# Optimization experiments

Measured on AMD Instinct MI355X. Metric: run time of the kernel, lower is better.

## Reference

```python
import jax, jax.numpy as jnp
import numpy as np

BATCH, NBITS = 32768, 512


def setup_inputs() -> dict:
    key = jax.random.key(0)
    raw = jax.random.randint(key, (BATCH, NBITS), 0, 2)
    bits = raw.astype(jnp.float32) * 2.0 - 1.0  # values in {-1, +1}
    return {"bits": bits}


def _joint_prob(b):
    # b in {0,1}, shape [B, N]. p_ij[i,j,m,n] = mean_b 1[b_i==m] * 1[b_j==n]
    B = b.shape[0]
    ind = jnp.stack([(b == 0.0), (b == 1.0)], axis=0).astype(b.dtype)  # [2, B, N]
    return jnp.einsum('mbi,nbj->ijmn', ind, ind) / B  # [N, N, 2, 2]


def reference(bits):
    b = bits / 2.0 + 0.5
    N = b.shape[1]
    p_ij = _joint_prob(b)
    p_i_pos = b.mean(axis=0)
    p_i = jnp.stack([1.0 - p_i_pos, p_i_pos], axis=-1)  # [N, 2]
    outer = p_i[:, None, :, None] * p_i[None, :, None, :]  # [N, N, 2, 2]
    ii = jnp.arange(N)
    tri = (ii[:, None] > ii[None, :])[:, :, None, None]  # triangle: keep i > j
    valid = tri & (p_ij > 0) & (p_i[:, None, :, None] > 0) & (p_i[None, :, None, :] > 0)
    safe_p = jnp.where(valid, p_ij, 1.0)
    safe_o = jnp.where(valid, outer, 1.0)
    terms = jnp.where(valid, safe_p * jnp.log(safe_p / safe_o), 0.0)
    cnt = valid.sum().astype(bits.dtype)
    return terms.sum() / cnt
```

## Files before the change

kernel.cpp:

```cpp
#include <hip/hip_runtime.h>
#include <stdint.h>

#define BATCH   32768
#define NBITS   512
#define NWORDS  512
#define NSLICE  32
#define SW      16
#define NTILE   36

typedef unsigned long long u64;

__global__ __launch_bounds__(256) void pack_kernel(const float* __restrict__ bits,
                                                   u64* __restrict__ packed,
                                                   double* __restrict__ lg,
                                                   int* __restrict__ c1) {
    const int gid = blockIdx.x * 256 + threadIdx.x;

    if (gid <= BATCH) lg[gid] = (gid > 0) ? log((double)gid) : 0.0;
    if (gid < NBITS) c1[gid] = 0;

    const int wv   = threadIdx.x >> 6;
    const int lane = threadIdx.x & 63;
    const int gw   = blockIdx.x * 4 + wv;
    const int w    = gw >> 2;
    const int q    = gw & 3;
    const int c0   = q * 128 + lane * 2;

    u64 m0 = 0, m1 = 0;
    const float* base = bits + (size_t)w * 64 * NBITS + c0;
#pragma unroll 16
    for (int r = 0; r < 64; ++r) {
        float2 v = *reinterpret_cast<const float2*>(base + (size_t)r * NBITS);
        const u64 b = 1ull << r;
        if (v.x > 0.0f) m0 |= b;
        if (v.y > 0.0f) m1 |= b;
    }
    ulonglong2 st; st.x = m0; st.y = m1;
    *reinterpret_cast<ulonglong2*>(&packed[(size_t)w * NBITS + c0]) = st;
}

__global__ __launch_bounds__(256) void gram_kernel(const u64* __restrict__ packed,
                                                   int* __restrict__ Cp,
                                                   int* __restrict__ c1) {
    __shared__ u64 ldsI[SW][64];
    __shared__ u64 ldsJ[SW][64];

    const int s = blockIdx.x & (NSLICE - 1);
    const int t = blockIdx.x >> 5;
    int bi = (int)((sqrtf(8.0f * (float)t + 1.0f) - 1.0f) * 0.5f);
    while ((bi + 1) * (bi + 2) / 2 <= t) ++bi;
    while (bi * (bi + 1) / 2 > t) --bi;
    const int bj = t - bi * (bi + 1) / 2;

    const int i0 = bi * 64, j0 = bj * 64;
    const int w0 = s * SW;
    const bool diag = (bi == bj);

    for (int q = threadIdx.x; q < SW * 32; q += 256) {
        const int wo = q >> 5, cp = (q & 31) * 2;
        const size_t g = (size_t)(w0 + wo) * NBITS;
        *reinterpret_cast<ulonglong2*>(&ldsI[wo][cp]) =
            *reinterpret_cast<const ulonglong2*>(&packed[g + i0 + cp]);
        if (!diag)
            *reinterpret_cast<ulonglong2*>(&ldsJ[wo][cp]) =
                *reinterpret_cast<const ulonglong2*>(&packed[g + j0 + cp]);
    }
    __syncthreads();

    const int tj2 = (threadIdx.x & 15) * 2;
    const int ti2 = (threadIdx.x >> 4) * 2;
    const u64 (*BJ)[64] = diag ? ldsI : ldsJ;

    int acc[4][4] = {};
#pragma unroll
    for (int w = 0; w < SW; ++w) {
        const u64 a0 = ldsI[w][ti2],      a1 = ldsI[w][ti2 + 1];
        const u64 a2 = ldsI[w][ti2 + 32], a3 = ldsI[w][ti2 + 33];
        const u64 b0 = BJ[w][tj2],        b1 = BJ[w][tj2 + 1];
        const u64 b2 = BJ[w][tj2 + 32],   b3 = BJ[w][tj2 + 33];
        acc[0][0] += __popcll(a0 & b0); acc[0][1] += __popcll(a0 & b1);
        acc[0][2] += __popcll(a0 & b2); acc[0][3] += __popcll(a0 & b3);
        acc[1][0] += __popcll(a1 & b0); acc[1][1] += __popcll(a1 & b1);
        acc[1][2] += __popcll(a1 & b2); acc[1][3] += __popcll(a1 & b3);
        acc[2][0] += __popcll(a2 & b0); acc[2][1] += __popcll(a2 & b1);
        acc[2][2] += __popcll(a2 & b2); acc[2][3] += __popcll(a2 & b3);
        acc[3][0] += __popcll(a3 & b0); acc[3][1] += __popcll(a3 & b1);
        acc[3][2] += __popcll(a3 & b2); acc[3][3] += __popcll(a3 & b3);
    }

    int* out = Cp + (size_t)s * NBITS * NBITS;
    const int io[4] = {ti2, ti2 + 1, ti2 + 32, ti2 + 33};
#pragma unroll
    for (int a = 0; a < 4; ++a) {
        const size_t row = (size_t)(i0 + io[a]) * NBITS + j0;
        *reinterpret_cast<int2*>(&out[row + tj2])      = make_int2(acc[a][0], acc[a][1]);
        *reinterpret_cast<int2*>(&out[row + tj2 + 32]) = make_int2(acc[a][2], acc[a][3]);
    }

    if (diag && ti2 == tj2) {
#pragma unroll
        for (int a = 0; a < 4; ++a)
            atomicAdd(&c1[i0 + io[a]], acc[a][a]);
    }
}

__global__ __launch_bounds__(256) void mi_kernel(const int* __restrict__ Cp,
                                                 const int* __restrict__ c1,
                                                 const double* __restrict__ lg,
                                                 double* __restrict__ bsum,
                                                 int* __restrict__ bcnt) {
    const double invB = 1.0 / (double)BATCH;
    const int i = blockIdx.x;
    const int ci = c1[i];
    const double lgB = lg[BATCH];
    double lsum = 0.0;
    int lcnt = 0;

#pragma unroll
    for (int half = 0; half < 2; ++half) {
        const int j = half * 256 + threadIdx.x;
        if (j < i) {
            int n11 = 0;
#pragma unroll
            for (int s = 0; s < NSLICE; ++s)
                n11 += Cp[(size_t)s * NBITS * NBITS + (size_t)i * NBITS + j];
            const int cj = c1[j];

            const int pim[2] = {BATCH - ci, ci};
            const int pjn[2] = {BATCH - cj, cj};
            const int nmn[2][2] = {{BATCH - ci - cj + n11, cj - n11},
                                   {ci - n11, n11}};
#pragma unroll
            for (int m = 0; m < 2; ++m)
#pragma unroll
                for (int n = 0; n < 2; ++n) {
                    const int c_mn = nmn[m][n];
                    if (c_mn > 0 && pim[m] > 0 && pjn[n] > 0) {
                        lsum += (double)c_mn * invB *
                                (lg[c_mn] + lgB - lg[pim[m]] - lg[pjn[n]]);
                        ++lcnt;
                    }
                }
        }
    }

    __shared__ double ssum[256];
    __shared__ int scnt[256];
    ssum[threadIdx.x] = lsum;
    scnt[threadIdx.x] = lcnt;
    __syncthreads();
    for (int off = 128; off > 0; off >>= 1) {
        if (threadIdx.x < off) {
            ssum[threadIdx.x] += ssum[threadIdx.x + off];
            scnt[threadIdx.x] += scnt[threadIdx.x + off];
        }
        __syncthreads();
    }
    if (threadIdx.x == 0) { bsum[blockIdx.x] = ssum[0]; bcnt[blockIdx.x] = scnt[0]; }
}

__global__ __launch_bounds__(256) void final_kernel(const double* __restrict__ bsum,
                                                    const int* __restrict__ bcnt,
                                                    float* __restrict__ out,
                                                    int nblocks) {
    __shared__ double ssum[256];
    __shared__ int scnt[256];
    double s = 0.0; int c = 0;
    for (int k = threadIdx.x; k < nblocks; k += 256) { s += bsum[k]; c += bcnt[k]; }
    ssum[threadIdx.x] = s;
    scnt[threadIdx.x] = c;
    __syncthreads();
    for (int off = 128; off > 0; off >>= 1) {
        if (threadIdx.x < off) {
            ssum[threadIdx.x] += ssum[threadIdx.x + off];
            scnt[threadIdx.x] += scnt[threadIdx.x + off];
        }
        __syncthreads();
    }
    if (threadIdx.x == 0) out[0] = (float)(ssum[0] / (double)scnt[0]);
}

extern "C" void kernel_launch(void* const* d_in, const int* in_sizes, int n_in,
                              void* d_out, int out_size, void* d_ws, size_t ws_size,
                              hipStream_t stream) {
    const float* bits = (const float*)d_in[0];
    char* ws = (char*)d_ws;
    u64*    packed = (u64*)ws;
    int*    Cp     = (int*)(ws + (2u << 20));
    double* lg     = (double*)(ws + (34u << 20));
    int*    c1     = (int*)(ws + (34u << 20) + (512u << 10));
    double* bsum   = (double*)(ws + (34u << 20) + (576u << 10));
    int*    bcnt   = (int*)(ws + (34u << 20) + (640u << 10));

    pack_kernel<<<512, 256, 0, stream>>>(bits, packed, lg, c1);
    gram_kernel<<<NTILE * NSLICE, 256, 0, stream>>>(packed, Cp, c1);
    mi_kernel<<<NBITS, 256, 0, stream>>>(Cp, c1, lg, bsum, bcnt);
    final_kernel<<<1, 256, 0, stream>>>(bsum, bcnt, (float*)d_out, NBITS);
}
```

Before: 43.55 us.

## Retile gram kernel to 32x32 single-wave blocks and fuse final reduction

```diff
diff --git a/kernel.cpp b/kernel.cpp
--- a/kernel.cpp
+++ b/kernel.cpp
@@ -4,20 +4,23 @@
 #define BATCH   32768
 #define NBITS   512
 #define NWORDS  512
-#define NSLICE  32
-#define SW      16
-#define NTILE   36
+#define NSLICE  16
+#define SW      32
+#define NT32    136
+#define MIGRID  512
 
 typedef unsigned long long u64;
 
 __global__ __launch_bounds__(256) void pack_kernel(const float* __restrict__ bits,
                                                    u64* __restrict__ packed,
                                                    double* __restrict__ lg,
-                                                   int* __restrict__ c1) {
+                                                   int* __restrict__ c1,
+                                                   int* __restrict__ done) {
     const int gid = blockIdx.x * 256 + threadIdx.x;
 
     if (gid <= BATCH) lg[gid] = (gid > 0) ? log((double)gid) : 0.0;
     if (gid < NBITS) c1[gid] = 0;
+    if (gid == NBITS) *done = 0;
 
     const int wv   = threadIdx.x >> 6;
     const int lane = threadIdx.x & 63;
@@ -39,25 +42,25 @@
     *reinterpret_cast<ulonglong2*>(&packed[(size_t)w * NBITS + c0]) = st;
 }
 
-__global__ __launch_bounds__(256) void gram_kernel(const u64* __restrict__ packed,
-                                                   int* __restrict__ Cp,
-                                                   int* __restrict__ c1) {
-    __shared__ u64 ldsI[SW][64];
-    __shared__ u64 ldsJ[SW][64];
+__global__ __launch_bounds__(64) void gram_kernel(const u64* __restrict__ packed,
+                                                  int* __restrict__ Cp,
+                                                  int* __restrict__ c1) {
+    __shared__ u64 ldsI[SW][32];
+    __shared__ u64 ldsJ[SW][32];
 
     const int s = blockIdx.x & (NSLICE - 1);
-    const int t = blockIdx.x >> 5;
+    const int t = blockIdx.x >> 4;
     int bi = (int)((sqrtf(8.0f * (float)t + 1.0f) - 1.0f) * 0.5f);
     while ((bi + 1) * (bi + 2) / 2 <= t) ++bi;
     while (bi * (bi + 1) / 2 > t) --bi;
     const int bj = t - bi * (bi + 1) / 2;
 
-    const int i0 = bi * 64, j0 = bj * 64;
+    const int i0 = bi * 32, j0 = bj * 32;
     const int w0 = s * SW;
     const bool diag = (bi == bj);
 
-    for (int q = threadIdx.x; q < SW * 32; q += 256) {
-        const int wo = q >> 5, cp = (q & 31) * 2;
+    for (int q = threadIdx.x; q < SW * 16; q += 64) {
+        const int wo = q >> 4, cp = (q & 15) * 2;
         const size_t g = (size_t)(w0 + wo) * NBITS;
         *reinterpret_cast<ulonglong2*>(&ldsI[wo][cp]) =
             *reinterpret_cast<const ulonglong2*>(&packed[g + i0 + cp]);
@@ -67,17 +70,17 @@
     }
     __syncthreads();
 
-    const int tj2 = (threadIdx.x & 15) * 2;
-    const int ti2 = (threadIdx.x >> 4) * 2;
-    const u64 (*BJ)[64] = diag ? ldsI : ldsJ;
+    const int tx4 = (threadIdx.x & 7) * 4;
+    const int ty4 = (threadIdx.x >> 3) * 4;
+    const u64 (*BJ)[32] = diag ? ldsI : ldsJ;
 
     int acc[4][4] = {};
-#pragma unroll
+#pragma unroll 4
     for (int w = 0; w < SW; ++w) {
-        const u64 a0 = ldsI[w][ti2],      a1 = ldsI[w][ti2 + 1];
-        const u64 a2 = ldsI[w][ti2 + 32], a3 = ldsI[w][ti2 + 33];
-        const u64 b0 = BJ[w][tj2],        b1 = BJ[w][tj2 + 1];
-        const u64 b2 = BJ[w][tj2 + 32],   b3 = BJ[w][tj2 + 33];
+        const u64 a0 = ldsI[w][ty4],     a1 = ldsI[w][ty4 + 1];
+        const u64 a2 = ldsI[w][ty4 + 2], a3 = ldsI[w][ty4 + 3];
+        const u64 b0 = BJ[w][tx4],       b1 = BJ[w][tx4 + 1];
+        const u64 b2 = BJ[w][tx4 + 2],   b3 = BJ[w][tx4 + 3];
         acc[0][0] += __popcll(a0 & b0); acc[0][1] += __popcll(a0 & b1);
         acc[0][2] += __popcll(a0 & b2); acc[0][3] += __popcll(a0 & b3);
         acc[1][0] += __popcll(a1 & b0); acc[1][1] += __popcll(a1 & b1);
@@ -89,18 +92,15 @@
     }
 
     int* out = Cp + (size_t)s * NBITS * NBITS;
-    const int io[4] = {ti2, ti2 + 1, ti2 + 32, ti2 + 33};
-#pragma unroll
-    for (int a = 0; a < 4; ++a) {
-        const size_t row = (size_t)(i0 + io[a]) * NBITS + j0;
-        *reinterpret_cast<int2*>(&out[row + tj2])      = make_int2(acc[a][0], acc[a][1]);
-        *reinterpret_cast<int2*>(&out[row + tj2 + 32]) = make_int2(acc[a][2], acc[a][3]);
-    }
-
-    if (diag && ti2 == tj2) {
+#pragma unroll
+    for (int a = 0; a < 4; ++a)
+        *reinterpret_cast<int4*>(&out[(size_t)(i0 + ty4 + a) * NBITS + j0 + tx4]) =
+            make_int4(acc[a][0], acc[a][1], acc[a][2], acc[a][3]);
+
+    if (diag && tx4 == ty4) {
 #pragma unroll
         for (int a = 0; a < 4; ++a)
-            atomicAdd(&c1[i0 + io[a]], acc[a][a]);
+            atomicAdd(&c1[i0 + ty4 + a], acc[a][a]);
     }
 }
 
@@ -108,7 +108,9 @@
                                                  const int* __restrict__ c1,
                                                  const double* __restrict__ lg,
                                                  double* __restrict__ bsum,
-                                                 int* __restrict__ bcnt) {
+                                                 int* __restrict__ bcnt,
+                                                 int* __restrict__ done,
+                                                 float* __restrict__ out) {
     const double invB = 1.0 / (double)BATCH;
     const int i = blockIdx.x;
     const int ci = c1[i];
@@ -146,6 +148,7 @@
 
     __shared__ double ssum[256];
     __shared__ int scnt[256];
+    __shared__ int lastFlag;
     ssum[threadIdx.x] = lsum;
     scnt[threadIdx.x] = lcnt;
     __syncthreads();
@@ -156,19 +159,21 @@
         }
         __syncthreads();
     }
-    if (threadIdx.x == 0) { bsum[blockIdx.x] = ssum[0]; bcnt[blockIdx.x] = scnt[0]; }
-}
-
-__global__ __launch_bounds__(256) void final_kernel(const double* __restrict__ bsum,
-                                                    const int* __restrict__ bcnt,
-                                                    float* __restrict__ out,
-                                                    int nblocks) {
-    __shared__ double ssum[256];
-    __shared__ int scnt[256];
-    double s = 0.0; int c = 0;
-    for (int k = threadIdx.x; k < nblocks; k += 256) { s += bsum[k]; c += bcnt[k]; }
-    ssum[threadIdx.x] = s;
-    scnt[threadIdx.x] = c;
+    if (threadIdx.x == 0) {
+        bsum[i] = ssum[0];
+        bcnt[i] = scnt[0];
+        __threadfence();
+        lastFlag = (atomicAdd(done, 1) == MIGRID - 1);
+    }
+    __syncthreads();
+    if (!lastFlag) return;
+
+    __threadfence();
+    double s2 = bsum[threadIdx.x] + bsum[threadIdx.x + 256];
+    int c2 = bcnt[threadIdx.x] + bcnt[threadIdx.x + 256];
+    __syncthreads();
+    ssum[threadIdx.x] = s2;
+    scnt[threadIdx.x] = c2;
     __syncthreads();
     for (int off = 128; off > 0; off >>= 1) {
         if (threadIdx.x < off) {
@@ -187,13 +192,13 @@
     char* ws = (char*)d_ws;
     u64*    packed = (u64*)ws;
     int*    Cp     = (int*)(ws + (2u << 20));
-    double* lg     = (double*)(ws + (34u << 20));
-    int*    c1     = (int*)(ws + (34u << 20) + (512u << 10));
-    double* bsum   = (double*)(ws + (34u << 20) + (576u << 10));
-    int*    bcnt   = (int*)(ws + (34u << 20) + (640u << 10));
-
-    pack_kernel<<<512, 256, 0, stream>>>(bits, packed, lg, c1);
-    gram_kernel<<<NTILE * NSLICE, 256, 0, stream>>>(packed, Cp, c1);
-    mi_kernel<<<NBITS, 256, 0, stream>>>(Cp, c1, lg, bsum, bcnt);
-    final_kernel<<<1, 256, 0, stream>>>(bsum, bcnt, (float*)d_out, NBITS);
-}
+    double* lg     = (double*)(ws + (18u << 20));
+    int*    c1     = (int*)(ws + (18u << 20) + (512u << 10));
+    int*    done   = (int*)(ws + (18u << 20) + (516u << 10));
+    double* bsum   = (double*)(ws + (18u << 20) + (576u << 10));
+    int*    bcnt   = (int*)(ws + (18u << 20) + (640u << 10));
+
+    pack_kernel<<<512, 256, 0, stream>>>(bits, packed, lg, c1, done);
+    gram_kernel<<<NT32 * NSLICE, 64, 0, stream>>>(packed, Cp, c1);
+    mi_kernel<<<MIGRID, 256, 0, stream>>>(Cp, c1, lg, bsum, bcnt, done, (float*)d_out);
+}
```

After: 50.60 us. 1.16x slower.

## Fuse pipeline into one persistent kernel with grid barriers and 16-bit partials

Applied to the files above, without the earlier changes.

```diff
diff --git a/kernel.cpp b/kernel.cpp
--- a/kernel.cpp
+++ b/kernel.cpp
@@ -7,123 +7,179 @@
 #define NSLICE  32
 #define SW      16
 #define NTILE   36
+#define NTASK   (NTILE * NSLICE)
+#define NBLK    256
+#define NTHR    512
 
 typedef unsigned long long u64;
 
-__global__ __launch_bounds__(256) void pack_kernel(const float* __restrict__ bits,
-                                                   u64* __restrict__ packed,
-                                                   double* __restrict__ lg,
-                                                   int* __restrict__ c1) {
-    const int gid = blockIdx.x * 256 + threadIdx.x;
+struct Ctrl { int cnt; int gen; int done; int pad; };
+
+__device__ inline void gbar(int* cnt, int* gen) {
+    __syncthreads();
+    if (threadIdx.x == 0) {
+        __threadfence();
+        const int g = atomicAdd(gen, 0);
+        const int old = atomicAdd(cnt, 1);
+        if (old == NBLK - 1) {
+            atomicExch(cnt, 0);
+            __threadfence();
+            atomicAdd(gen, 1);
+        } else {
+            while (atomicAdd(gen, 0) == g) __builtin_amdgcn_s_sleep(8);
+        }
+        __threadfence();
+    }
+    __syncthreads();
+}
+
+__global__ __launch_bounds__(NTHR, 2) void fused_kernel(
+    const float* __restrict__ bits,
+    u64* __restrict__ packed,
+    unsigned short* __restrict__ Cp,
+    double* __restrict__ lg,
+    int* __restrict__ c1,
+    Ctrl* __restrict__ ctrl,
+    double* __restrict__ bsum,
+    int* __restrict__ bcnt,
+    float* __restrict__ out)
+{
+    __shared__ u64 lds[2][2][SW][64];
+    __shared__ double ssum[NTHR];
+    __shared__ int scnt[NTHR];
+    __shared__ int lastFlag;
+
+    const int tid = threadIdx.x;
+    const int b   = blockIdx.x;
+    const int gid = b * NTHR + tid;
 
     if (gid <= BATCH) lg[gid] = (gid > 0) ? log((double)gid) : 0.0;
-    if (gid < NBITS) c1[gid] = 0;
-
-    const int wv   = threadIdx.x >> 6;
-    const int lane = threadIdx.x & 63;
-    const int gw   = blockIdx.x * 4 + wv;
-    const int w    = gw >> 2;
-    const int q    = gw & 3;
-    const int c0   = q * 128 + lane * 2;
-
-    u64 m0 = 0, m1 = 0;
-    const float* base = bits + (size_t)w * 64 * NBITS + c0;
+    if (gid < NBITS)  c1[gid] = 0;
+
+    {
+        const int wid  = tid >> 6;
+        const int lane = tid & 63;
+        const int gw   = b * 8 + wid;
+        const int w    = gw >> 2;
+        const int q    = gw & 3;
+        const int c0   = q * 128 + lane * 2;
+
+        u64 m0 = 0, m1 = 0;
+        const float* base = bits + (size_t)w * 64 * NBITS + c0;
 #pragma unroll 16
-    for (int r = 0; r < 64; ++r) {
-        float2 v = *reinterpret_cast<const float2*>(base + (size_t)r * NBITS);
-        const u64 b = 1ull << r;
-        if (v.x > 0.0f) m0 |= b;
-        if (v.y > 0.0f) m1 |= b;
-    }
-    ulonglong2 st; st.x = m0; st.y = m1;
-    *reinterpret_cast<ulonglong2*>(&packed[(size_t)w * NBITS + c0]) = st;
-}
-
-__global__ __launch_bounds__(256) void gram_kernel(const u64* __restrict__ packed,
-                                                   int* __restrict__ Cp,
-                                                   int* __restrict__ c1) {
-    __shared__ u64 ldsI[SW][64];
-    __shared__ u64 ldsJ[SW][64];
-
-    const int s = blockIdx.x & (NSLICE - 1);
-    const int t = blockIdx.x >> 5;
-    int bi = (int)((sqrtf(8.0f * (float)t + 1.0f) - 1.0f) * 0.5f);
-    while ((bi + 1) * (bi + 2) / 2 <= t) ++bi;
-    while (bi * (bi + 1) / 2 > t) --bi;
-    const int bj = t - bi * (bi + 1) / 2;
-
-    const int i0 = bi * 64, j0 = bj * 64;
-    const int w0 = s * SW;
-    const bool diag = (bi == bj);
-
-    for (int q = threadIdx.x; q < SW * 32; q += 256) {
-        const int wo = q >> 5, cp = (q & 31) * 2;
-        const size_t g = (size_t)(w0 + wo) * NBITS;
-        *reinterpret_cast<ulonglong2*>(&ldsI[wo][cp]) =
-            *reinterpret_cast<const ulonglong2*>(&packed[g + i0 + cp]);
-        if (!diag)
-            *reinterpret_cast<ulonglong2*>(&ldsJ[wo][cp]) =
-                *reinterpret_cast<const ulonglong2*>(&packed[g + j0 + cp]);
-    }
-    __syncthreads();
-
-    const int tj2 = (threadIdx.x & 15) * 2;
-    const int ti2 = (threadIdx.x >> 4) * 2;
-    const u64 (*BJ)[64] = diag ? ldsI : ldsJ;
-
-    int acc[4][4] = {};
-#pragma unroll
-    for (int w = 0; w < SW; ++w) {
-        const u64 a0 = ldsI[w][ti2],      a1 = ldsI[w][ti2 + 1];
-        const u64 a2 = ldsI[w][ti2 + 32], a3 = ldsI[w][ti2 + 33];
-        const u64 b0 = BJ[w][tj2],        b1 = BJ[w][tj2 + 1];
-        const u64 b2 = BJ[w][tj2 + 32],   b3 = BJ[w][tj2 + 33];
-        acc[0][0] += __popcll(a0 & b0); acc[0][1] += __popcll(a0 & b1);
-        acc[0][2] += __popcll(a0 & b2); acc[0][3] += __popcll(a0 & b3);
-        acc[1][0] += __popcll(a1 & b0); acc[1][1] += __popcll(a1 & b1);
-        acc[1][2] += __popcll(a1 & b2); acc[1][3] += __popcll(a1 & b3);
-        acc[2][0] += __popcll(a2 & b0); acc[2][1] += __popcll(a2 & b1);
-        acc[2][2] += __popcll(a2 & b2); acc[2][3] += __popcll(a2 & b3);
-        acc[3][0] += __popcll(a3 & b0); acc[3][1] += __popcll(a3 & b1);
-        acc[3][2] += __popcll(a3 & b2); acc[3][3] += __popcll(a3 & b3);
-    }
-
-    int* out = Cp + (size_t)s * NBITS * NBITS;
-    const int io[4] = {ti2, ti2 + 1, ti2 + 32, ti2 + 33};
-#pragma unroll
-    for (int a = 0; a < 4; ++a) {
-        const size_t row = (size_t)(i0 + io[a]) * NBITS + j0;
-        *reinterpret_cast<int2*>(&out[row + tj2])      = make_int2(acc[a][0], acc[a][1]);
-        *reinterpret_cast<int2*>(&out[row + tj2 + 32]) = make_int2(acc[a][2], acc[a][3]);
-    }
-
-    if (diag && ti2 == tj2) {
-#pragma unroll
-        for (int a = 0; a < 4; ++a)
-            atomicAdd(&c1[i0 + io[a]], acc[a][a]);
-    }
-}
-
-__global__ __launch_bounds__(256) void mi_kernel(const int* __restrict__ Cp,
-                                                 const int* __restrict__ c1,
-                                                 const double* __restrict__ lg,
-                                                 double* __restrict__ bsum,
-                                                 int* __restrict__ bcnt) {
+        for (int r = 0; r < 64; ++r) {
+            float2 v = *reinterpret_cast<const float2*>(base + (size_t)r * NBITS);
+            const u64 bb = 1ull << r;
+            if (v.x > 0.0f) m0 |= bb;
+            if (v.y > 0.0f) m1 |= bb;
+        }
+        ulonglong2 st; st.x = m0; st.y = m1;
+        *reinterpret_cast<ulonglong2*>(&packed[(size_t)w * NBITS + c0]) = st;
+    }
+
+    gbar(&ctrl->cnt, &ctrl->gen);
+
+    {
+        const int grp = tid >> 8;
+        const int gt  = tid & 255;
+        const int gg  = b * 2 + grp;
+
+        for (int it = 0; it < 3; ++it) {
+            const int task = gg + it * 512;
+            int i0 = 0, j0 = 0, w0 = 0;
+            bool diag = false;
+            const bool active = (task < NTASK);
+            if (active) {
+                const int s = task & (NSLICE - 1);
+                const int t = task >> 5;
+                int bi = (int)((sqrtf(8.0f * (float)t + 1.0f) - 1.0f) * 0.5f);
+                while ((bi + 1) * (bi + 2) / 2 <= t) ++bi;
+                while (bi * (bi + 1) / 2 > t) --bi;
+                const int bj = t - bi * (bi + 1) / 2;
+                i0 = bi * 64; j0 = bj * 64; w0 = (task & (NSLICE - 1)) * SW;
+                diag = (bi == bj);
+                (void)s;
+
+                for (int q2 = gt; q2 < SW * 32; q2 += 256) {
+                    const int wo = q2 >> 5, cp = (q2 & 31) * 2;
+                    const size_t g = (size_t)(w0 + wo) * NBITS;
+                    *reinterpret_cast<ulonglong2*>(&lds[grp][0][wo][cp]) =
+                        *reinterpret_cast<const ulonglong2*>(&packed[g + i0 + cp]);
+                    if (!diag)
+                        *reinterpret_cast<ulonglong2*>(&lds[grp][1][wo][cp]) =
+                            *reinterpret_cast<const ulonglong2*>(&packed[g + j0 + cp]);
+                }
+            }
+            __syncthreads();
+            if (active) {
+                const int tj2 = (gt & 15) * 2;
+                const int ti2 = (gt >> 4) * 2;
+                const u64 (*LI)[64] = lds[grp][0];
+                const u64 (*LJ)[64] = diag ? lds[grp][0] : lds[grp][1];
+
+                int acc[4][4] = {};
+#pragma unroll
+                for (int w = 0; w < SW; ++w) {
+                    const u64 a0 = LI[w][ti2],      a1 = LI[w][ti2 + 1];
+                    const u64 a2 = LI[w][ti2 + 32], a3 = LI[w][ti2 + 33];
+                    const u64 b0 = LJ[w][tj2],      b1 = LJ[w][tj2 + 1];
+                    const u64 b2 = LJ[w][tj2 + 32], b3 = LJ[w][tj2 + 33];
+                    acc[0][0] += __popcll(a0 & b0); acc[0][1] += __popcll(a0 & b1);
+                    acc[0][2] += __popcll(a0 & b2); acc[0][3] += __popcll(a0 & b3);
+                    acc[1][0] += __popcll(a1 & b0); acc[1][1] += __popcll(a1 & b1);
+                    acc[1][2] += __popcll(a1 & b2); acc[1][3] += __popcll(a1 & b3);
+                    acc[2][0] += __popcll(a2 & b0); acc[2][1] += __popcll(a2 & b1);
+                    acc[2][2] += __popcll(a2 & b2); acc[2][3] += __popcll(a2 & b3);
+                    acc[3][0] += __popcll(a3 & b0); acc[3][1] += __popcll(a3 & b1);
+                    acc[3][2] += __popcll(a3 & b2); acc[3][3] += __popcll(a3 & b3);
+                }
+
+                unsigned short* cs = Cp + ((size_t)(task & (NSLICE - 1)) << 18);
+                const int io[4] = {ti2, ti2 + 1, ti2 + 32, ti2 + 33};
+#pragma unroll
+                for (int a = 0; a < 4; ++a) {
+                    const size_t row = (size_t)(i0 + io[a]) * NBITS + j0;
+                    ushort2 u;
+                    u.x = (unsigned short)acc[a][0]; u.y = (unsigned short)acc[a][1];
+                    *reinterpret_cast<ushort2*>(&cs[row + tj2]) = u;
+                    u.x = (unsigned short)acc[a][2]; u.y = (unsigned short)acc[a][3];
+                    *reinterpret_cast<ushort2*>(&cs[row + tj2 + 32]) = u;
+                }
+                if (diag && ti2 == tj2) {
+#pragma unroll
+                    for (int a = 0; a < 4; ++a)
+                        atomicAdd(&c1[i0 + io[a]], acc[a][a]);
+                }
+            }
+            __syncthreads();
+        }
+    }
+
+    gbar(&ctrl->cnt, &ctrl->gen);
+
     const double invB = 1.0 / (double)BATCH;
-    const int i = blockIdx.x;
-    const int ci = c1[i];
-    const double lgB = lg[BATCH];
+    const double lgB  = lg[BATCH];
     double lsum = 0.0;
     int lcnt = 0;
 
-#pragma unroll
-    for (int half = 0; half < 2; ++half) {
-        const int j = half * 256 + threadIdx.x;
-        if (j < i) {
+    {
+        int i, jlist[2]; int nj = 0;
+        if (tid < 256) {
+            i = b;
+            if (tid < i) jlist[nj++] = tid;
+        } else {
+            i = 511 - b;
+            const int jj = tid - 256;
+            if (jj < i)       jlist[nj++] = jj;
+            if (jj + 256 < i) jlist[nj++] = jj + 256;
+        }
+        const int ci = c1[i];
+        for (int k = 0; k < nj; ++k) {
+            const int j = jlist[k];
             int n11 = 0;
 #pragma unroll
             for (int s = 0; s < NSLICE; ++s)
-                n11 += Cp[(size_t)s * NBITS * NBITS + (size_t)i * NBITS + j];
+                n11 += Cp[((size_t)s << 18) + (size_t)i * NBITS + j];
             const int cj = c1[j];
 
             const int pim[2] = {BATCH - ci, ci};
@@ -144,40 +200,36 @@
         }
     }
 
-    __shared__ double ssum[256];
-    __shared__ int scnt[256];
-    ssum[threadIdx.x] = lsum;
-    scnt[threadIdx.x] = lcnt;
+    ssum[tid] = lsum;
+    scnt[tid] = lcnt;
+    __syncthreads();
+    for (int off = 256; off > 0; off >>= 1) {
+        if (tid < off) {
+            ssum[tid] += ssum[tid + off];
+            scnt[tid] += scnt[tid + off];
+        }
+        __syncthreads();
+    }
+    if (tid == 0) {
+        bsum[b] = ssum[0];
+        bcnt[b] = scnt[0];
+        __threadfence();
+        lastFlag = (atomicAdd(&ctrl->done, 1) == NBLK - 1);
+    }
+    __syncthreads();
+    if (!lastFlag) return;
+
+    __threadfence();
+    if (tid < 256) { ssum[tid] = bsum[tid]; scnt[tid] = bcnt[tid]; }
     __syncthreads();
     for (int off = 128; off > 0; off >>= 1) {
-        if (threadIdx.x < off) {
-            ssum[threadIdx.x] += ssum[threadIdx.x + off];
-            scnt[threadIdx.x] += scnt[threadIdx.x + off];
+        if (tid < off) {
+            ssum[tid] += ssum[tid + off];
+            scnt[tid] += scnt[tid + off];
         }
         __syncthreads();
     }
-    if (threadIdx.x == 0) { bsum[blockIdx.x] = ssum[0]; bcnt[blockIdx.x] = scnt[0]; }
-}
-
-__global__ __launch_bounds__(256) void final_kernel(const double* __restrict__ bsum,
-                                                    const int* __restrict__ bcnt,
-                                                    float* __restrict__ out,
-                                                    int nblocks) {
-    __shared__ double ssum[256];
-    __shared__ int scnt[256];
-    double s = 0.0; int c = 0;
-    for (int k = threadIdx.x; k < nblocks; k += 256) { s += bsum[k]; c += bcnt[k]; }
-    ssum[threadIdx.x] = s;
-    scnt[threadIdx.x] = c;
-    __syncthreads();
-    for (int off = 128; off > 0; off >>= 1) {
-        if (threadIdx.x < off) {
-            ssum[threadIdx.x] += ssum[threadIdx.x + off];
-            scnt[threadIdx.x] += scnt[threadIdx.x + off];
-        }
-        __syncthreads();
-    }
-    if (threadIdx.x == 0) out[0] = (float)(ssum[0] / (double)scnt[0]);
+    if (tid == 0) out[0] = (float)(ssum[0] / (double)scnt[0]);
 }
 
 extern "C" void kernel_launch(void* const* d_in, const int* in_sizes, int n_in,
@@ -185,15 +237,15 @@
                               hipStream_t stream) {
     const float* bits = (const float*)d_in[0];
     char* ws = (char*)d_ws;
-    u64*    packed = (u64*)ws;
-    int*    Cp     = (int*)(ws + (2u << 20));
-    double* lg     = (double*)(ws + (34u << 20));
-    int*    c1     = (int*)(ws + (34u << 20) + (512u << 10));
-    double* bsum   = (double*)(ws + (34u << 20) + (576u << 10));
-    int*    bcnt   = (int*)(ws + (34u << 20) + (640u << 10));
-
-    pack_kernel<<<512, 256, 0, stream>>>(bits, packed, lg, c1);
-    gram_kernel<<<NTILE * NSLICE, 256, 0, stream>>>(packed, Cp, c1);
-    mi_kernel<<<NBITS, 256, 0, stream>>>(Cp, c1, lg, bsum, bcnt);
-    final_kernel<<<1, 256, 0, stream>>>(bsum, bcnt, (float*)d_out, NBITS);
+    u64*            packed = (u64*)ws;
+    unsigned short* Cp     = (unsigned short*)(ws + (2u << 20));
+    double*         lg     = (double*)(ws + (18u << 20));
+    int*            c1     = (int*)(ws + (18u << 20) + (512u << 10));
+    Ctrl*           ctrl   = (Ctrl*)(ws + (18u << 20) + (516u << 10));
+    double*         bsum   = (double*)(ws + (18u << 20) + (520u << 10));
+    int*            bcnt   = (int*)(ws + (18u << 20) + (524u << 10));
+
+    hipMemsetAsync(ctrl, 0, sizeof(Ctrl), stream);
+    fused_kernel<<<NBLK, NTHR, 0, stream>>>(bits, packed, Cp, lg, c1, ctrl,
+                                            bsum, bcnt, (float*)d_out);
 }
```

Result: slower. 99.53 us (+128.6%).

## Store partial Gram counts as uint16 and fuse final reduction via last-block atomic

Applied to the files above, without the earlier changes.

```diff
diff --git a/kernel.cpp b/kernel.cpp
--- a/kernel.cpp
+++ b/kernel.cpp
@@ -7,17 +7,20 @@
 #define NSLICE  32
 #define SW      16
 #define NTILE   36
+#define MIGRID  512
 
 typedef unsigned long long u64;
 
 __global__ __launch_bounds__(256) void pack_kernel(const float* __restrict__ bits,
                                                    u64* __restrict__ packed,
                                                    double* __restrict__ lg,
-                                                   int* __restrict__ c1) {
+                                                   int* __restrict__ c1,
+                                                   int* __restrict__ done) {
     const int gid = blockIdx.x * 256 + threadIdx.x;
 
     if (gid <= BATCH) lg[gid] = (gid > 0) ? log((double)gid) : 0.0;
     if (gid < NBITS) c1[gid] = 0;
+    if (gid == NBITS) *done = 0;
 
     const int wv   = threadIdx.x >> 6;
     const int lane = threadIdx.x & 63;
@@ -40,7 +43,7 @@
 }
 
 __global__ __launch_bounds__(256) void gram_kernel(const u64* __restrict__ packed,
-                                                   int* __restrict__ Cp,
+                                                   unsigned short* __restrict__ Cp,
                                                    int* __restrict__ c1) {
     __shared__ u64 ldsI[SW][64];
     __shared__ u64 ldsJ[SW][64];
@@ -88,13 +91,16 @@
         acc[3][2] += __popcll(a3 & b2); acc[3][3] += __popcll(a3 & b3);
     }
 
-    int* out = Cp + (size_t)s * NBITS * NBITS;
+    unsigned short* out = Cp + ((size_t)s << 18);
     const int io[4] = {ti2, ti2 + 1, ti2 + 32, ti2 + 33};
 #pragma unroll
     for (int a = 0; a < 4; ++a) {
         const size_t row = (size_t)(i0 + io[a]) * NBITS + j0;
-        *reinterpret_cast<int2*>(&out[row + tj2])      = make_int2(acc[a][0], acc[a][1]);
-        *reinterpret_cast<int2*>(&out[row + tj2 + 32]) = make_int2(acc[a][2], acc[a][3]);
+        ushort2 u;
+        u.x = (unsigned short)acc[a][0]; u.y = (unsigned short)acc[a][1];
+        *reinterpret_cast<ushort2*>(&out[row + tj2]) = u;
+        u.x = (unsigned short)acc[a][2]; u.y = (unsigned short)acc[a][3];
+        *reinterpret_cast<ushort2*>(&out[row + tj2 + 32]) = u;
     }
 
     if (diag && ti2 == tj2) {
@@ -104,11 +110,13 @@
     }
 }
 
-__global__ __launch_bounds__(256) void mi_kernel(const int* __restrict__ Cp,
+__global__ __launch_bounds__(256) void mi_kernel(const unsigned short* __restrict__ Cp,
                                                  const int* __restrict__ c1,
                                                  const double* __restrict__ lg,
                                                  double* __restrict__ bsum,
-                                                 int* __restrict__ bcnt) {
+                                                 int* __restrict__ bcnt,
+                                                 int* __restrict__ done,
+                                                 float* __restrict__ out) {
     const double invB = 1.0 / (double)BATCH;
     const int i = blockIdx.x;
     const int ci = c1[i];
@@ -123,7 +131,7 @@
             int n11 = 0;
 #pragma unroll
             for (int s = 0; s < NSLICE; ++s)
-                n11 += Cp[(size_t)s * NBITS * NBITS + (size_t)i * NBITS + j];
+                n11 += Cp[((size_t)s << 18) + (size_t)i * NBITS + j];
             const int cj = c1[j];
 
             const int pim[2] = {BATCH - ci, ci};
@@ -146,6 +154,7 @@
 
     __shared__ double ssum[256];
     __shared__ int scnt[256];
+    __shared__ int lastFlag;
     ssum[threadIdx.x] = lsum;
     scnt[threadIdx.x] = lcnt;
     __syncthreads();
@@ -156,19 +165,21 @@
         }
         __syncthreads();
     }
-    if (threadIdx.x == 0) { bsum[blockIdx.x] = ssum[0]; bcnt[blockIdx.x] = scnt[0]; }
-}
-
-__global__ __launch_bounds__(256) void final_kernel(const double* __restrict__ bsum,
-                                                    const int* __restrict__ bcnt,
-                                                    float* __restrict__ out,
-                                                    int nblocks) {
-    __shared__ double ssum[256];
-    __shared__ int scnt[256];
-    double s = 0.0; int c = 0;
-    for (int k = threadIdx.x; k < nblocks; k += 256) { s += bsum[k]; c += bcnt[k]; }
-    ssum[threadIdx.x] = s;
-    scnt[threadIdx.x] = c;
+    if (threadIdx.x == 0) {
+        bsum[i] = ssum[0];
+        bcnt[i] = scnt[0];
+        __threadfence();
+        lastFlag = (atomicAdd(done, 1) == MIGRID - 1);
+    }
+    __syncthreads();
+    if (!lastFlag) return;
+
+    __threadfence();
+    double s2 = bsum[threadIdx.x] + bsum[threadIdx.x + 256];
+    int c2 = bcnt[threadIdx.x] + bcnt[threadIdx.x + 256];
+    __syncthreads();
+    ssum[threadIdx.x] = s2;
+    scnt[threadIdx.x] = c2;
     __syncthreads();
     for (int off = 128; off > 0; off >>= 1) {
         if (threadIdx.x < off) {
@@ -185,15 +196,15 @@
                               hipStream_t stream) {
     const float* bits = (const float*)d_in[0];
     char* ws = (char*)d_ws;
-    u64*    packed = (u64*)ws;
-    int*    Cp     = (int*)(ws + (2u << 20));
-    double* lg     = (double*)(ws + (34u << 20));
-    int*    c1     = (int*)(ws + (34u << 20) + (512u << 10));
-    double* bsum   = (double*)(ws + (34u << 20) + (576u << 10));
-    int*    bcnt   = (int*)(ws + (34u << 20) + (640u << 10));
-
-    pack_kernel<<<512, 256, 0, stream>>>(bits, packed, lg, c1);
+    u64*            packed = (u64*)ws;
+    unsigned short* Cp     = (unsigned short*)(ws + (2u << 20));
+    double*         lg     = (double*)(ws + (18u << 20));
+    int*            c1     = (int*)(ws + (18u << 20) + (512u << 10));
+    int*            done   = (int*)(ws + (18u << 20) + (516u << 10));
+    double*         bsum   = (double*)(ws + (18u << 20) + (576u << 10));
+    int*            bcnt   = (int*)(ws + (18u << 20) + (640u << 10));
+
+    pack_kernel<<<512, 256, 0, stream>>>(bits, packed, lg, c1, done);
     gram_kernel<<<NTILE * NSLICE, 256, 0, stream>>>(packed, Cp, c1);
-    mi_kernel<<<NBITS, 256, 0, stream>>>(Cp, c1, lg, bsum, bcnt);
-    final_kernel<<<1, 256, 0, stream>>>(bsum, bcnt, (float*)d_out, NBITS);
-}
+    mi_kernel<<<MIGRID, 256, 0, stream>>>(Cp, c1, lg, bsum, bcnt, done, (float*)d_out);
+}
```

Result: slower. 52.91 us (+21.5%).
